# Kernel optimization log

Measured on AMD Instinct MI355X. Metric: run time of the kernel, lower is better.

The kernel has to match this reference:

```python
import jax, jax.numpy as jnp
import numpy as np


def setup_inputs() -> dict:
    key = jax.random.key(0)
    ks = jax.random.split(key, 8)
    N, NL, C, E, P3, P2, P1 = 2048, 16, 128, 10, 23, 4, 1
    return {
        "x": jax.random.normal(ks[0], (N, NL, C), dtype=jnp.float32),
        "atom_types": jax.random.randint(ks[1], (N,), 0, E),
        "U3": jax.random.normal(ks[2], (NL, NL, NL, P3), dtype=jnp.float32),
        "U2": jax.random.normal(ks[3], (NL, NL, P2), dtype=jnp.float32),
        "U1": jax.random.normal(ks[4], (NL, P1), dtype=jnp.float32),
        "W3": jax.random.normal(ks[5], (E, P3, C), dtype=jnp.float32),
        "W2": jax.random.normal(ks[6], (E, P2, C), dtype=jnp.float32),
        "W1": jax.random.normal(ks[7], (E, P1, C), dtype=jnp.float32),
    }


def reference(x, atom_types, U3, U2, U1, W3, W2, W1):
    # MACE symmetric contraction, correlation order 3, per-atom-type weights.
    # x: [N, nl, C]; atom_types: [N]; U3: [nl,nl,nl,P3]; W3: [E,P3,C]; etc.
    w3 = W3[atom_types]  # [N, P3, C]
    w2 = W2[atom_types]  # [N, P2, C]
    w1 = W1[atom_types]  # [N, P1, C]
    # Correlation-3 term: c3[n,a,b,c] = sum_{i,k} U3[a,b,i,k] * w3[n,k,c] * x[n,i,c]
    xw = jnp.einsum('nkc,nic->nkic', w3, x)        # [N, P3, nl, C]
    c3 = jnp.einsum('abik,nkic->nabc', U3, xw)     # [N, nl, nl, C]
    # Add correlation-2 term, contract one nl index with x.
    c2 = c3 + jnp.einsum('abk,nkc->nabc', U2, w2)  # [N, nl, nl, C]
    c1 = jnp.einsum('nabc,nbc->nac', c2, x)        # [N, nl, C]
    # Add correlation-1 term, contract last nl index with x.
    c1 = c1 + jnp.einsum('ak,nkc->nac', U1, w1)    # [N, nl, C]
    out = jnp.einsum('nac,nac->nc', c1, x)         # [N, C]
    return out
```

## Files before the change

kernel.cpp:

```cpp
#include <hip/hip_runtime.h>


constexpr int NL = 16;
constexpr int CC = 128;
constexpr int EE = 10;
constexpr int P3 = 23;
constexpr int P2 = 4;
constexpr int P1 = 1;
constexpr int NTRI = 816;
constexpr int NPAIR = 136;
constexpr int GG = 4;
constexpr int ASPLIT = 4;

constexpr int pairsBefore(int a) {
    int s = 0;
    for (int x = 0; x < a; x++) s += NL - x;
    return s;
}
constexpr int trisBefore(int a) {
    int s = 0;
    for (int x = 0; x < a; x++) s += (NL - x) * (NL - x + 1) / 2;
    return s;
}
static_assert(trisBefore(ASPLIT) % 4 == 0, "tri split must be float4-aligned");
static_assert(pairsBefore(ASPLIT) % 2 == 0, "pair split must be float2-aligned");

__global__ void k_symU(const float* __restrict__ U3, const float* __restrict__ U2,
                       float* __restrict__ U3s, float* __restrict__ U2s) {
    int idx = blockIdx.x * blockDim.x + threadIdx.x;
    if (idx < NTRI * P3) {
        int tri = idx / P3, k = idx % P3;
        int rem = tri, a = 0;
        while (rem >= (NL - a) * (NL - a + 1) / 2) { rem -= (NL - a) * (NL - a + 1) / 2; a++; }
        int b = a;
        while (rem >= NL - b) { rem -= NL - b; b++; }
        int i = b + rem;
        auto u = [&](int p, int q, int r) { return U3[((p * NL + q) * NL + r) * P3 + k]; };
        float s = u(a,b,i) + u(a,i,b) + u(b,a,i) + u(b,i,a) + u(i,a,b) + u(i,b,a);
        int m = (a == b && b == i) ? 6 : ((a == b || b == i) ? 2 : 1);
        U3s[idx] = s / (float)m;
    } else if (idx < NTRI * P3 + NPAIR * P2) {
        int j = idx - NTRI * P3;
        int pr = j / P2, k = j % P2;
        int rem = pr, a = 0;
        while (rem >= NL - a) { rem -= NL - a; a++; }
        int b = a + rem;
        float s = U2[(a * NL + b) * P2 + k];
        if (a != b) s += U2[(b * NL + a) * P2 + k];
        U2s[pr * P2 + k] = s;
    }
}

__global__ void k_buildA(const float* __restrict__ U3s, const float* __restrict__ U2s,
                         const float* __restrict__ U1,
                         const float* __restrict__ W3, const float* __restrict__ W2,
                         const float* __restrict__ W1,
                         float* __restrict__ A3, float* __restrict__ A2, float* __restrict__ A1) {
    int b = blockIdx.x;
    int c = threadIdx.x;
    if (b < EE * NTRI) {
        int t = b / NTRI, tri = b % NTRI;
        float s = 0.f;
        #pragma unroll
        for (int k = 0; k < P3; k++) s += U3s[tri * P3 + k] * W3[(t * P3 + k) * CC + c];
        A3[(((size_t)t * (NTRI / 4) + (tri >> 2)) * CC + c) * 4 + (tri & 3)] = s;
    } else if (b < EE * (NTRI + NPAIR)) {
        int j = b - EE * NTRI;
        int t = j / NPAIR, pr = j % NPAIR;
        float s = 0.f;
        #pragma unroll
        for (int k = 0; k < P2; k++) s += U2s[pr * P2 + k] * W2[(t * P2 + k) * CC + c];
        A2[(((size_t)t * (NPAIR / 2) + (pr >> 1)) * CC + c) * 2 + (pr & 1)] = s;
    } else {
        int t = b - EE * (NTRI + NPAIR);
        for (int a = 0; a < NL; a++) {
            float s = 0.f;
            #pragma unroll
            for (int k = 0; k < P1; k++) s += U1[a * P1 + k] * W1[(t * P1 + k) * CC + c];
            A1[((size_t)t * NL + a) * CC + c] = s;
        }
    }
}

__global__ void k_zero(int* counts) {
    if (threadIdx.x < 16) counts[threadIdx.x] = 0;
}

__global__ void k_bucket(const int* __restrict__ types, int* counts, int* buckets, int N) {
    int n = blockIdx.x * blockDim.x + threadIdx.x;
    if (n < N) {
        int t = types[n];
        int pos = atomicAdd(&counts[t], 1);
        buckets[t * N + pos] = n;
    }
}

__global__ void k_groups(const int* __restrict__ counts, const int* __restrict__ buckets,
                         int* __restrict__ groups, int* __restrict__ ngroups, int N) {
    __shared__ int goff[EE + 1];
    if (threadIdx.x == 0) {
        int off = 0;
        for (int t = 0; t < EE; t++) { goff[t] = off; off += (counts[t] + GG - 1) / GG; }
        goff[EE] = off;
        *ngroups = off;
    }
    __syncthreads();
    for (int t = 0; t < EE; t++) {
        int cnt = counts[t];
        int ng = (cnt + GG - 1) / GG;
        for (int g = threadIdx.x; g < ng; g += blockDim.x) {
            int* gr = &groups[(goff[t] + g) * 8];
            int nv = cnt - g * GG; if (nv > GG) nv = GG;
            gr[0] = t;
            gr[5] = nv;
            for (int j = 0; j < GG; j++) {
                int jj = j < nv ? j : nv - 1;
                gr[1 + j] = buckets[t * N + g * GG + jj];
            }
        }
    }
}

template <int A0, int A1, bool LIN>
__device__ __forceinline__ void eval_nest(const float (&xv)[GG][NL],
                                          const float4* __restrict__ a3v,
                                          const float2* __restrict__ a2v,
                                          const float* __restrict__ a1p,
                                          float (&acc)[GG]) {
    if (LIN) {
        #pragma unroll
        for (int a = 0; a < NL; a++) {
            float w = a1p[a * CC];
            #pragma unroll
            for (int g = 0; g < GG; g++) acc[g] += w * xv[g][a];
        }
    }
    float4 w4 = {0.f, 0.f, 0.f, 0.f};
    float2 wp = {0.f, 0.f};
    int tri = trisBefore(A0), pr = pairsBefore(A0);
    #pragma unroll
    for (int a = A0; a < A1; a++) {
        #pragma unroll
        for (int b = a; b < NL; b++) {
            float p[GG];
            #pragma unroll
            for (int g = 0; g < GG; g++) p[g] = xv[g][a] * xv[g][b];
            if ((pr & 1) == 0) wp = a2v[(size_t)(pr >> 1) * CC];
            float w2 = ((pr & 1) == 0) ? wp.x : wp.y;
            pr++;
            #pragma unroll
            for (int g = 0; g < GG; g++) acc[g] += w2 * p[g];
            #pragma unroll
            for (int i = b; i < NL; i++) {
                if ((tri & 3) == 0) w4 = a3v[(size_t)(tri >> 2) * CC];
                int r = tri & 3;
                float w3 = (r == 0) ? w4.x : (r == 1) ? w4.y : (r == 2) ? w4.z : w4.w;
                tri++;
                #pragma unroll
                for (int g = 0; g < GG; g++) acc[g] += w3 * (p[g] * xv[g][i]);
            }
        }
    }
}

__global__ __launch_bounds__(CC, 3) void k_main(const float* __restrict__ x,
                                                const float* __restrict__ A3,
                                                const float* __restrict__ A2,
                                                const float* __restrict__ A1,
                                                const int* __restrict__ groups,
                                                const int* __restrict__ ngroups,
                                                float* __restrict__ out) {
    int blk = blockIdx.x;
    if (blk >= *ngroups) return;
    const int* gr = groups + blk * 8;
    int t = gr[0];
    int nvalid = gr[5];
    int c = threadIdx.x;

    int na[GG];
    #pragma unroll
    for (int g = 0; g < GG; g++) na[g] = gr[1 + g];

    float xv[GG][NL];
    #pragma unroll
    for (int g = 0; g < GG; g++)
        #pragma unroll
        for (int i = 0; i < NL; i++)
            xv[g][i] = x[((size_t)na[g] * NL + i) * CC + c];

    const float4* a3v = (const float4*)A3 + (size_t)t * (NTRI / 4) * CC + c;
    const float2* a2v = (const float2*)A2 + (size_t)t * (NPAIR / 2) * CC + c;
    const float* a1p = A1 + (size_t)t * NL * CC + c;

    float acc[GG] = {0.f, 0.f, 0.f, 0.f};
    if (blockIdx.y == 0)
        eval_nest<0, ASPLIT, true>(xv, a3v, a2v, a1p, acc);
    else
        eval_nest<ASPLIT, NL, false>(xv, a3v, a2v, a1p, acc);

    #pragma unroll
    for (int g = 0; g < GG; g++)
        if (g < nvalid) atomicAdd(&out[(size_t)na[g] * CC + c], acc[g]);
}

extern "C" void kernel_launch(void* const* d_in, const int* in_sizes, int n_in,
                              void* d_out, int out_size, void* d_ws, size_t ws_size,
                              hipStream_t stream) {
    const float* x   = (const float*)d_in[0];
    const int* types = (const int*)d_in[1];
    const float* U3  = (const float*)d_in[2];
    const float* U2  = (const float*)d_in[3];
    const float* U1  = (const float*)d_in[4];
    const float* W3  = (const float*)d_in[5];
    const float* W2  = (const float*)d_in[6];
    const float* W1  = (const float*)d_in[7];
    float* out = (float*)d_out;
    int N = in_sizes[1];

    int ngmax = (N + GG - 1) / GG + EE;

    float* ws   = (float*)d_ws;
    float* U3s  = ws;
    float* U2s  = U3s + NTRI * P3;
    float* A3   = U2s + NPAIR * P2;
    float* A2   = A3 + (size_t)EE * NTRI * CC;
    float* A1   = A2 + (size_t)EE * NPAIR * CC;
    int* counts  = (int*)(A1 + (size_t)EE * NL * CC);
    int* buckets = counts + 16;
    int* groups  = buckets + (size_t)EE * N;
    int* ngroups = groups + (size_t)ngmax * 8;

    hipMemsetAsync(out, 0, (size_t)out_size * sizeof(float), stream);

    int symThreads = NTRI * P3 + NPAIR * P2;
    hipLaunchKernelGGL(k_symU, dim3((symThreads + 255) / 256), dim3(256), 0, stream,
                       U3, U2, U3s, U2s);
    hipLaunchKernelGGL(k_buildA, dim3(EE * (NTRI + NPAIR) + EE), dim3(CC), 0, stream,
                       U3s, U2s, U1, W3, W2, W1, A3, A2, A1);
    hipLaunchKernelGGL(k_zero, dim3(1), dim3(64), 0, stream, counts);
    hipLaunchKernelGGL(k_bucket, dim3((N + 255) / 256), dim3(256), 0, stream,
                       types, counts, buckets, N);
    hipLaunchKernelGGL(k_groups, dim3(1), dim3(256), 0, stream,
                       counts, buckets, groups, ngroups, N);
    hipLaunchKernelGGL(k_main, dim3(ngmax, 2), dim3(CC), 0, stream,
                       x, A3, A2, A1, groups, ngroups, out);
}
```

Baseline: 127.4 us.

## Factor contraction nest, raise group size to 6, split a-range four ways, fuse setup kernels

The main kernel now factors the symmetric contraction Horner-style, accumulating the inner i-sum into r, then multiplying by x_b and x_a. This cuts the multiplies per triple and avoids recomputing pair products. Atoms per group rise from 4 to 6, and the a-range is split across four grid-y slices instead of two, with each slice loading only the x entries it needs. Setup is consolidated: the out and counts zeroing moves into k_symU, replacing the memset and k_zero, and k_buildA is restructured around shared-memory tiles with fewer, larger blocks. Costs include more register pressure from GG=6, uneven work across the four splits, and more atomic adds into out.

New measurement: 190.5 us. +49.5%, slower.

```diff
diff --git a/kernel.cpp b/kernel.cpp
--- a/kernel.cpp
+++ b/kernel.cpp
@@ -6,11 +6,9 @@
 constexpr int EE = 10;
 constexpr int P3 = 23;
 constexpr int P2 = 4;
-constexpr int P1 = 1;
 constexpr int NTRI = 816;
 constexpr int NPAIR = 136;
-constexpr int GG = 4;
-constexpr int ASPLIT = 4;
+constexpr int GG = 6;
 
 constexpr int pairsBefore(int a) {
     int s = 0;
@@ -22,12 +20,16 @@
     for (int x = 0; x < a; x++) s += (NL - x) * (NL - x + 1) / 2;
     return s;
 }
-static_assert(trisBefore(ASPLIT) % 4 == 0, "tri split must be float4-aligned");
-static_assert(pairsBefore(ASPLIT) % 2 == 0, "pair split must be float2-aligned");
+static_assert(trisBefore(2) % 4 == 0 && trisBefore(4) % 4 == 0 && trisBefore(8) % 4 == 0, "");
 
 __global__ void k_symU(const float* __restrict__ U3, const float* __restrict__ U2,
-                       float* __restrict__ U3s, float* __restrict__ U2s) {
-    int idx = blockIdx.x * blockDim.x + threadIdx.x;
+                       float* __restrict__ U3s, float* __restrict__ U2s,
+                       float* __restrict__ out, int out_n, int* __restrict__ counts) {
+    int gtid = blockIdx.x * blockDim.x + threadIdx.x;
+    int nthreads = gridDim.x * blockDim.x;
+    if (gtid < 16) counts[gtid] = 0;
+    for (int idx = gtid; idx < out_n; idx += nthreads) out[idx] = 0.f;
+    int idx = gtid;
     if (idx < NTRI * P3) {
         int tri = idx / P3, k = idx % P3;
         int rem = tri, a = 0;
@@ -51,39 +53,51 @@
     }
 }
 
-__global__ void k_buildA(const float* __restrict__ U3s, const float* __restrict__ U2s,
-                         const float* __restrict__ U1,
-                         const float* __restrict__ W3, const float* __restrict__ W2,
-                         const float* __restrict__ W1,
-                         float* __restrict__ A3, float* __restrict__ A2, float* __restrict__ A1) {
-    int b = blockIdx.x;
-    int c = threadIdx.x;
-    if (b < EE * NTRI) {
-        int t = b / NTRI, tri = b % NTRI;
-        float s = 0.f;
-        #pragma unroll
-        for (int k = 0; k < P3; k++) s += U3s[tri * P3 + k] * W3[(t * P3 + k) * CC + c];
-        A3[(((size_t)t * (NTRI / 4) + (tri >> 2)) * CC + c) * 4 + (tri & 3)] = s;
-    } else if (b < EE * (NTRI + NPAIR)) {
-        int j = b - EE * NTRI;
-        int t = j / NPAIR, pr = j % NPAIR;
-        float s = 0.f;
-        #pragma unroll
-        for (int k = 0; k < P2; k++) s += U2s[pr * P2 + k] * W2[(t * P2 + k) * CC + c];
-        A2[(((size_t)t * (NPAIR / 2) + (pr >> 1)) * CC + c) * 2 + (pr & 1)] = s;
+__global__ __launch_bounds__(256) void k_buildA(const float* __restrict__ U3s,
+                                                const float* __restrict__ U2s,
+                                                const float* __restrict__ U1,
+                                                const float* __restrict__ W3,
+                                                const float* __restrict__ W2,
+                                                const float* __restrict__ W1,
+                                                float* __restrict__ A3, float* __restrict__ A2,
+                                                float* __restrict__ A1) {
+    int blk = blockIdx.x;
+    int tid = threadIdx.x;
+    if (blk < EE * 8) {
+        int t = blk / 8, chunk = blk % 8;
+        __shared__ float W3s[P3 * CC];
+        __shared__ float U3c[102 * P3];
+        for (int idx = tid; idx < P3 * CC; idx += 256) W3s[idx] = W3[t * P3 * CC + idx];
+        for (int idx = tid; idx < 102 * P3; idx += 256) U3c[idx] = U3s[chunk * 102 * P3 + idx];
+        __syncthreads();
+        int c = tid & 127, h = tid >> 7;
+        for (int j = 0; j < 51; j++) {
+            int tsub = h * 51 + j;
+            int tri = chunk * 102 + tsub;
+            float s = 0.f;
+            #pragma unroll
+            for (int k = 0; k < P3; k++) s += U3c[tsub * P3 + k] * W3s[k * CC + c];
+            A3[(((size_t)t * (NTRI / 4) + (tri >> 2)) * CC + c) * 4 + (tri & 3)] = s;
+        }
     } else {
-        int t = b - EE * (NTRI + NPAIR);
-        for (int a = 0; a < NL; a++) {
+        int t = blk - EE * 8;
+        __shared__ float W2s[P2 * CC];
+        __shared__ float U2c[NPAIR * P2];
+        for (int idx = tid; idx < P2 * CC; idx += 256) W2s[idx] = W2[t * P2 * CC + idx];
+        for (int idx = tid; idx < NPAIR * P2; idx += 256) U2c[idx] = U2s[idx];
+        __syncthreads();
+        int c = tid & 127, h = tid >> 7;
+        for (int j = 0; j < NPAIR / 2; j++) {
+            int pr = h * (NPAIR / 2) + j;
             float s = 0.f;
             #pragma unroll
-            for (int k = 0; k < P1; k++) s += U1[a * P1 + k] * W1[(t * P1 + k) * CC + c];
-            A1[((size_t)t * NL + a) * CC + c] = s;
-        }
-    }
-}
-
-__global__ void k_zero(int* counts) {
-    if (threadIdx.x < 16) counts[threadIdx.x] = 0;
+            for (int k = 0; k < P2; k++) s += U2c[pr * P2 + k] * W2s[k * CC + c];
+            A2[((size_t)t * NPAIR + pr) * CC + c] = s;
+        }
+        if (h == 0)
+            for (int a = 0; a < NL; a++)
+                A1[((size_t)t * NL + a) * CC + c] = U1[a] * W1[t * CC + c];
+    }
 }
 
 __global__ void k_bucket(const int* __restrict__ types, int* counts, int* buckets, int N) {
@@ -112,7 +126,7 @@
             int* gr = &groups[(goff[t] + g) * 8];
             int nv = cnt - g * GG; if (nv > GG) nv = GG;
             gr[0] = t;
-            gr[5] = nv;
+            gr[7] = nv;
             for (int j = 0; j < GG; j++) {
                 int jj = j < nv ? j : nv - 1;
                 gr[1 + j] = buckets[t * N + g * GG + jj];
@@ -121,12 +135,20 @@
     }
 }
 
-template <int A0, int A1, bool LIN>
-__device__ __forceinline__ void eval_nest(const float (&xv)[GG][NL],
+template <int A0, int A1v, bool LIN>
+__device__ __forceinline__ void run_split(const float* __restrict__ x,
                                           const float4* __restrict__ a3v,
-                                          const float2* __restrict__ a2v,
+                                          const float* __restrict__ a2p,
                                           const float* __restrict__ a1p,
-                                          float (&acc)[GG]) {
+                                          const int (&na)[GG], int c, float (&acc)[GG]) {
+    float xv[GG][NL];
+    constexpr int L0 = LIN ? 0 : A0;
+    #pragma unroll
+    for (int g = 0; g < GG; g++)
+        #pragma unroll
+        for (int i = L0; i < NL; i++)
+            xv[g][i] = x[((size_t)na[g] * NL + i) * CC + c];
+
     if (LIN) {
         #pragma unroll
         for (int a = 0; a < NL; a++) {
@@ -135,31 +157,34 @@
             for (int g = 0; g < GG; g++) acc[g] += w * xv[g][a];
         }
     }
+
     float4 w4 = {0.f, 0.f, 0.f, 0.f};
-    float2 wp = {0.f, 0.f};
     int tri = trisBefore(A0), pr = pairsBefore(A0);
     #pragma unroll
-    for (int a = A0; a < A1; a++) {
+    for (int a = A0; a < A1v; a++) {
+        float s[GG];
+        #pragma unroll
+        for (int g = 0; g < GG; g++) s[g] = 0.f;
         #pragma unroll
         for (int b = a; b < NL; b++) {
-            float p[GG];
-            #pragma unroll
-            for (int g = 0; g < GG; g++) p[g] = xv[g][a] * xv[g][b];
-            if ((pr & 1) == 0) wp = a2v[(size_t)(pr >> 1) * CC];
-            float w2 = ((pr & 1) == 0) ? wp.x : wp.y;
-            pr++;
-            #pragma unroll
-            for (int g = 0; g < GG; g++) acc[g] += w2 * p[g];
+            float w2 = a2p[(size_t)pr * CC]; pr++;
+            float r[GG];
+            #pragma unroll
+            for (int g = 0; g < GG; g++) r[g] = w2;
             #pragma unroll
             for (int i = b; i < NL; i++) {
                 if ((tri & 3) == 0) w4 = a3v[(size_t)(tri >> 2) * CC];
-                int r = tri & 3;
-                float w3 = (r == 0) ? w4.x : (r == 1) ? w4.y : (r == 2) ? w4.z : w4.w;
+                int rr = tri & 3;
+                float w3 = (rr == 0) ? w4.x : (rr == 1) ? w4.y : (rr == 2) ? w4.z : w4.w;
                 tri++;
                 #pragma unroll
-                for (int g = 0; g < GG; g++) acc[g] += w3 * (p[g] * xv[g][i]);
+                for (int g = 0; g < GG; g++) r[g] += w3 * xv[g][i];
             }
-        }
+            #pragma unroll
+            for (int g = 0; g < GG; g++) s[g] += xv[g][b] * r[g];
+        }
+        #pragma unroll
+        for (int g = 0; g < GG; g++) acc[g] += xv[g][a] * s[g];
     }
 }
 
@@ -174,29 +199,24 @@
     if (blk >= *ngroups) return;
     const int* gr = groups + blk * 8;
     int t = gr[0];
-    int nvalid = gr[5];
+    int nvalid = gr[7];
     int c = threadIdx.x;
 
     int na[GG];
     #pragma unroll
     for (int g = 0; g < GG; g++) na[g] = gr[1 + g];
 
-    float xv[GG][NL];
-    #pragma unroll
-    for (int g = 0; g < GG; g++)
-        #pragma unroll
-        for (int i = 0; i < NL; i++)
-            xv[g][i] = x[((size_t)na[g] * NL + i) * CC + c];
-
     const float4* a3v = (const float4*)A3 + (size_t)t * (NTRI / 4) * CC + c;
-    const float2* a2v = (const float2*)A2 + (size_t)t * (NPAIR / 2) * CC + c;
+    const float* a2p = A2 + (size_t)t * NPAIR * CC + c;
     const float* a1p = A1 + (size_t)t * NL * CC + c;
 
-    float acc[GG] = {0.f, 0.f, 0.f, 0.f};
-    if (blockIdx.y == 0)
-        eval_nest<0, ASPLIT, true>(xv, a3v, a2v, a1p, acc);
-    else
-        eval_nest<ASPLIT, NL, false>(xv, a3v, a2v, a1p, acc);
+    float acc[GG] = {0.f, 0.f, 0.f, 0.f, 0.f, 0.f};
+    switch (blockIdx.y) {
+        case 0: run_split<0, 2, true >(x, a3v, a2p, a1p, na, c, acc); break;
+        case 1: run_split<2, 4, false>(x, a3v, a2p, a1p, na, c, acc); break;
+        case 2: run_split<4, 8, false>(x, a3v, a2p, a1p, na, c, acc); break;
+        default: run_split<8, 16, false>(x, a3v, a2p, a1p, na, c, acc); break;
+    }
 
     #pragma unroll
     for (int g = 0; g < GG; g++)
@@ -230,18 +250,14 @@
     int* groups  = buckets + (size_t)EE * N;
     int* ngroups = groups + (size_t)ngmax * 8;
 
-    hipMemsetAsync(out, 0, (size_t)out_size * sizeof(float), stream);
-
-    int symThreads = NTRI * P3 + NPAIR * P2;
-    hipLaunchKernelGGL(k_symU, dim3((symThreads + 255) / 256), dim3(256), 0, stream,
-                       U3, U2, U3s, U2s);
-    hipLaunchKernelGGL(k_buildA, dim3(EE * (NTRI + NPAIR) + EE), dim3(CC), 0, stream,
+    hipLaunchKernelGGL(k_symU, dim3(76), dim3(256), 0, stream,
+                       U3, U2, U3s, U2s, out, out_size, counts);
+    hipLaunchKernelGGL(k_buildA, dim3(EE * 8 + EE), dim3(256), 0, stream,
                        U3s, U2s, U1, W3, W2, W1, A3, A2, A1);
-    hipLaunchKernelGGL(k_zero, dim3(1), dim3(64), 0, stream, counts);
     hipLaunchKernelGGL(k_bucket, dim3((N + 255) / 256), dim3(256), 0, stream,
                        types, counts, buckets, N);
     hipLaunchKernelGGL(k_groups, dim3(1), dim3(256), 0, stream,
                        counts, buckets, groups, ngroups, N);
-    hipLaunchKernelGGL(k_main, dim3(ngmax, 2), dim3(CC), 0, stream,
+    hipLaunchKernelGGL(k_main, dim3(ngmax, 4), dim3(CC), 0, stream,
                        x, A3, A2, A1, groups, ngroups, out);
 }
```
